# Performance work log

Measured on AMD Instinct MI355X. Metric: run time of the kernel, lower is better.

Reference implementation:

```python
import jax, jax.numpy as jnp
import numpy as np

N = 200000
B = 2
GX, GY, GZ = 480, 360, 32          # full-res voxel grid for input_coords
GX2, GY2, GZ2 = 240, 180, 16       # output_scale grid for bxyz_indx
CIN, CR, COUT = 64, 64, 64
CR2 = CR // 2
P_SCALE = (2, 4, 6, 8)


def setup_inputs() -> dict:
    key = jax.random.key(0)
    ks = jax.random.split(key, 24)
    s = 0.05
    input_data = jax.random.normal(ks[0], (N, CIN), dtype=jnp.float32)
    bcol = jax.random.randint(ks[1], (N, 1), 0, B, dtype=jnp.int32)
    xc = jax.random.randint(ks[2], (N, 1), 0, GX, dtype=jnp.int32)
    yc = jax.random.randint(ks[3], (N, 1), 0, GY, dtype=jnp.int32)
    zc = jax.random.randint(ks[4], (N, 1), 0, GZ, dtype=jnp.int32)
    input_coords = jnp.concatenate([bcol, xc, yc, zc], axis=1)
    input_coords_inv = jax.random.randint(ks[5], (N,), 0, N, dtype=jnp.int32)
    b2 = jax.random.randint(ks[6], (N, 1), 0, B, dtype=jnp.int32)
    x2 = jax.random.randint(ks[7], (N, 1), 0, GX2, dtype=jnp.int32)
    y2 = jax.random.randint(ks[8], (N, 1), 0, GY2, dtype=jnp.int32)
    z2 = jax.random.randint(ks[9], (N, 1), 0, GZ2, dtype=jnp.int32)
    bxyz_indx = jnp.concatenate([b2, x2, y2, z2], axis=1)
    # parameters (torch Linear stored here as [in, out])
    W_red = jax.random.normal(ks[10], (CIN, CR)) * s
    b_red = jnp.zeros((CR,), jnp.float32)
    fc_list_W = jax.random.normal(ks[11], (4, CR, CR2)) * s
    fc_list_b = jnp.zeros((4, CR2), jnp.float32)
    fcs_W = jax.random.normal(ks[12], (4, CR2, CR2)) * s
    fcs_b = jnp.zeros((4, CR2), jnp.float32)
    fc_W = jax.random.normal(ks[13], (CR2, CR2)) * s
    out_fc_W = jax.random.normal(ks[14], (CR2, CR)) * s
    lo_W1 = jax.random.normal(ks[15], (2 * CR, CR)) * s
    lo_W2 = jax.random.normal(ks[16], (CR, COUT)) * s
    lo_b2 = jnp.zeros((COUT,), jnp.float32)
    return dict(input_data=input_data, input_coords=input_coords,
                input_coords_inv=input_coords_inv, bxyz_indx=bxyz_indx,
                W_red=W_red, b_red=b_red, fc_list_W=fc_list_W, fc_list_b=fc_list_b,
                fcs_W=fcs_W, fcs_b=fcs_b, fc_W=fc_W, out_fc_W=out_fc_W,
                lo_W1=lo_W1, lo_W2=lo_W2, lo_b2=lo_b2)


def _segment_mean(x, seg, num_segments):
    sums = jax.ops.segment_sum(x, seg, num_segments=num_segments)
    cnt = jax.ops.segment_sum(jnp.ones((x.shape[0], 1), x.dtype), seg,
                              num_segments=num_segments)
    return sums / jnp.maximum(cnt, 1.0)


def reference(input_data, input_coords, input_coords_inv, bxyz_indx,
              W_red, b_red, fc_list_W, fc_list_b, fcs_W, fcs_b,
              fc_W, out_fc_W, lo_W1, lo_W2, lo_b2):
    reduced = jax.nn.relu(input_data @ W_red + b_red)          # [N, CR]
    bcol = input_coords[:, 0]
    xyz = input_coords[:, 1:]
    outs = []
    for j, ps in enumerate(P_SCALE):
        dx = (GX - 1) // ps + 1
        dy = (GY - 1) // ps + 1
        dz = (GZ - 1) // ps + 1
        q = xyz // ps                                          # [N, 3]
        # dense linearized voxel id replaces torch.unique(return_inverse)
        lin = ((bcol * dx + q[:, 0]) * dy + q[:, 1]) * dz + q[:, 2]
        nseg = B * dx * dy * dz
        fkm = _segment_mean(reduced, lin, nseg)                # [nseg, CR]
        att = jax.nn.relu(fkm @ fc_list_W[j] + fc_list_b[j])   # [nseg, CR2]
        outs.append(att[lin])                                  # gather back [N, CR2]
    scale_features = jnp.stack(outs, axis=1)                   # [N, 4, CR2]
    feat_S = scale_features.sum(axis=1)                        # [N, CR2]
    feat_Z = jax.nn.relu(feat_S @ fc_W)                        # [N, CR2]
    att_v = jax.nn.sigmoid(jnp.einsum('nc,kcd->nkd', feat_Z, fcs_W) + fcs_b)
    fused = (scale_features * att_v).sum(axis=1) @ out_fc_W    # [N, CR]
    output_f = jnp.concatenate([reduced, fused], axis=1)       # [N, 2*CR]
    proj = jax.nn.relu(output_f @ lo_W1) @ lo_W2 + lo_b2       # [N, COUT]
    proj = proj[input_coords_inv]
    # with_fm branch: index = (b, z, y, x) of bxyz_indx (b,x,y,z)
    lin2 = ((bxyz_indx[:, 0] * GZ2 + bxyz_indx[:, 3]) * GY2
            + bxyz_indx[:, 2]) * GX2 + bxyz_indx[:, 1]
    tv_fmap = jax.ops.segment_max(proj, lin2, num_segments=B * GZ2 * GY2 * GX2)
    tv_fmap = jnp.where(jnp.isneginf(tv_fmap), 0.0, tv_fmap)   # empty voxels -> 0
    return proj, tv_fmap, lin2
```

## Files before the change

### kernel.cpp

```cpp
#include <hip/hip_runtime.h>
#include <math.h>

#define NPTS   200000
#define CR     64
#define CR2    32

#define NSEG0      1382400
#define SUM123_ROW2 172800
#define SUM123_ROW3 230400
#define SUM123_ROWS 252000

#define TVSEG  1382400
#define GX2    240
#define GY2    180
#define GZ2    16

#define NBATCH 21600

__device__ __forceinline__ float bcastf(float v, int l) {
    return __int_as_float(__builtin_amdgcn_readlane(__float_as_int(v), l));
}

__device__ __forceinline__ int lin_scale(int b, int x, int y, int z,
                                         int ps, int dx, int dy, int dz) {
    int qx = x / ps, qy = y / ps, qz = z / ps;
    return ((b * dx + qx) * dy + qy) * dz + qz;
}

__device__ __forceinline__ void seg_decode(int seg, int& l1, int& l2, int& l3) {
    int qz = seg & 15; int rest = seg >> 4;
    int qy = rest % 180; int rest2 = rest / 180;
    int qx = rest2 % 240; int bb = rest2 / 240;
    l1 = ((bb * 120 + (qx >> 1)) * 90 + (qy >> 1)) * 8 + (qz >> 1);
    l2 = ((bb *  80 + (qx / 3)) * 60 + (qy / 3)) * 6 + (qz / 3);
    l3 = ((bb *  60 + (qx >> 2)) * 45 + (qy >> 2)) * 4 + (qz >> 2);
}

__device__ __forceinline__ int gatt_child(int s, int lane) {
    if (s < SUM123_ROW2) {
        int qz = s & 7, t = s >> 3;
        int qy = t % 90, t2 = t / 90;
        int qx = t2 % 120, b = t2 / 120;
        if (lane >= 8) return -1;
        int i = (lane >> 2) & 1, j = (lane >> 1) & 1, k = lane & 1;
        return ((b * 240 + 2 * qx + i) * 180 + 2 * qy + j) * 16 + 2 * qz + k;
    } else if (s < SUM123_ROW3) {
        int s2 = s - SUM123_ROW2;
        int qz = s2 % 6, t = s2 / 6;
        int qy = t % 60, t2 = t / 60;
        int qx = t2 % 80, b = t2 / 80;
        if (lane >= 27) return -1;
        int i = lane / 9, j = (lane / 3) % 3, k = lane % 3;
        int cz = 3 * qz + k;
        if (cz >= 16) return -1;
        return ((b * 240 + 3 * qx + i) * 180 + 3 * qy + j) * 16 + cz;
    } else {
        int s3 = s - SUM123_ROW3;
        int qz = s3 & 3, t = s3 >> 2;
        int qy = t % 45, t2 = t / 45;
        int qx = t2 % 60, b = t2 / 60;
        int i = lane >> 4, j = (lane >> 2) & 3, k = lane & 3;
        return ((b * 240 + 4 * qx + i) * 180 + 4 * qy + j) * 16 + 4 * qz + k;
    }
}

__global__ __launch_bounds__(256) void k_redscat(
        const float* __restrict__ in, const int* __restrict__ coords,
        const float* __restrict__ Wred, const float* __restrict__ bred,
        float* __restrict__ red, float* __restrict__ sum0,
        float* __restrict__ cnt) {
    __shared__ float Wl[CR * CR];
    for (int i = threadIdx.x; i < CR * CR; i += blockDim.x) Wl[i] = Wred[i];
    __syncthreads();
    int lane = threadIdx.x & 63;
    float bl = bred[lane];
    int wid  = blockIdx.x * 4 + (threadIdx.x >> 6);
    int nw   = gridDim.x * 4;
    for (int p = wid; p < NPTS / 2; p += nw) {
        int r0 = 2 * p, r1 = r0 + 1;
        float x0 = in[(size_t)r0 * CR + lane];
        float x1 = in[(size_t)r1 * CR + lane];
        float acc0 = bl, acc1 = bl;
#pragma unroll
        for (int k = 0; k < CR; ++k) {
            float w = Wl[k * CR + lane];
            acc0 += bcastf(x0, k) * w;
            acc1 += bcastf(x1, k) * w;
        }
        acc0 = fmaxf(acc0, 0.f); acc1 = fmaxf(acc1, 0.f);
        red[(size_t)r0 * CR + lane] = acc0;
        red[(size_t)r1 * CR + lane] = acc1;
        int4 c0 = ((const int4*)coords)[r0];
        int4 c1 = ((const int4*)coords)[r1];
        int l0a = lin_scale(c0.x, c0.y, c0.z, c0.w, 2, 240, 180, 16);
        int l0b = lin_scale(c1.x, c1.y, c1.z, c1.w, 2, 240, 180, 16);
        atomicAdd(&sum0[(size_t)l0a * CR + lane], acc0);
        atomicAdd(&sum0[(size_t)l0b * CR + lane], acc1);
        if (lane == 0) {
            atomicAdd(&cnt[l0a], 1.0f);
            atomicAdd(&cnt[l0b], 1.0f);
        }
    }
}

__global__ __launch_bounds__(256) void k_gatt(
        const float* __restrict__ sum0, float* __restrict__ attbuf,
        const float* __restrict__ cnt,
        const float* __restrict__ fcW, const float* __restrict__ fcB,
        int* __restrict__ list0, int* __restrict__ listCount,
        int* __restrict__ rankArr,
        const float* __restrict__ outW, const float* __restrict__ loW1,
        float* __restrict__ M) {
    __shared__ float sw[3 * CR * CR2];
    __shared__ int s_wavecnt[4];
    __shared__ int s_base;

    if (blockIdx.x < 8) {
        int e = blockIdx.x * 256 + threadIdx.x;
        if (e < 2048) {
            int r = e >> 6, c = e & 63;
            float acc = 0.f;
#pragma unroll
            for (int k = 0; k < 64; ++k)
                acc += outW[r * 64 + k] * loW1[(64 + k) * 64 + c];
            M[e] = acc;
        }
        return;
    }
    if (blockIdx.x < 1088) {
        int lane = threadIdx.x & 63;
        int w = threadIdx.x >> 6;
        int batch0 = (blockIdx.x - 8) * 20 + w * 5;
        int mycount = 0;
        for (int b = 0; b < 5; ++b) {
            float c = cnt[(batch0 + b) * 64 + lane];
            unsigned long long mask = __ballot(c > 0.f);
            mycount += __popcll(mask);
        }
        if (lane == 0) s_wavecnt[w] = mycount;
        __syncthreads();
        if (threadIdx.x == 0) {
            int tot = s_wavecnt[0] + s_wavecnt[1] + s_wavecnt[2] + s_wavecnt[3];
            s_base = atomicAdd(listCount, tot);
        }
        __syncthreads();
        int offset = s_base;
        for (int ww = 0; ww < w; ++ww) offset += s_wavecnt[ww];
        for (int b = 0; b < 5; ++b) {
            int cell = (batch0 + b) * 64 + lane;
            float c = cnt[cell];
            unsigned long long mask = __ballot(c > 0.f);
            if (c > 0.f) {
                int my = offset + __popcll(mask & ((1ull << lane) - 1ull));
                list0[my] = cell;
                rankArr[cell] = my;
            }
            offset += __popcll(mask);
        }
        return;
    }

    for (int i = threadIdx.x; i < 3 * CR * CR2; i += blockDim.x)
        sw[i] = fcW[CR * CR2 + i];
    __syncthreads();
    int lane = threadIdx.x & 63;
    int d = lane & 31;
    int wid = (blockIdx.x - 1088) * 4 + (threadIdx.x >> 6);
    int nw  = 2048 * 4;
    for (int p = wid; p < SUM123_ROWS / 2; p += nw) {
        int s0 = 2 * p, s1 = s0 + 1;
        const float* w; float bj;
        if (s0 < SUM123_ROW2)      { w = sw;        bj = fcB[1 * CR2 + d]; }
        else if (s0 < SUM123_ROW3) { w = sw + 2048; bj = fcB[2 * CR2 + d]; }
        else                       { w = sw + 4096; bj = fcB[3 * CR2 + d]; }

        int cl0 = gatt_child(s0, lane);
        int cl1 = gatt_child(s1, lane);
        float c0 = (cl0 >= 0) ? cnt[cl0] : 0.f;
        float c1 = (cl1 >= 0) ? cnt[cl1] : 0.f;
        unsigned long long mask0 = __ballot(c0 > 0.f);
        unsigned long long mask1 = __ballot(c1 > 0.f);
        if (!(mask0 | mask1)) continue;
        float t0 = c0, t1 = c1;
#pragma unroll
        for (int sh = 1; sh <= 32; sh <<= 1) {
            t0 += __shfl_xor(t0, sh, 64);
            t1 += __shfl_xor(t1, sh, 64);
        }

        float acc0 = 0.f, acc1 = 0.f;
        if (s0 < SUM123_ROW2) {
            int qz = s0 & 7, t = s0 >> 3;
            int qy = t % 90, t2 = t / 90;
            int qx = t2 % 120, b = t2 / 120;
            int base0 = ((b * 240 + 2 * qx) * 180 + 2 * qy) * 16 + 2 * qz;
            int base1 = base0 + 2;
#pragma unroll
            for (int c = 0; c < 8; ++c) {
                int off = (c >> 2) * 2880 + ((c >> 1) & 1) * 16 + (c & 1);
                if (mask0 & (1ull << c)) acc0 += sum0[(size_t)(base0 + off) * CR + lane];
                if (mask1 & (1ull << c)) acc1 += sum0[(size_t)(base1 + off) * CR + lane];
            }
        } else if (s0 < SUM123_ROW3) {
            int s2 = s0 - SUM123_ROW2;
            int qz = s2 % 6, t = s2 / 6;
            int qy = t % 60, t2 = t / 60;
            int qx = t2 % 80, b = t2 / 80;
            int base0 = ((b * 240 + 3 * qx) * 180 + 3 * qy) * 16 + 3 * qz;
            int base1 = base0 + 3;
#pragma unroll
            for (int c = 0; c < 27; ++c) {
                int off = (c / 9) * 2880 + ((c / 3) % 3) * 16 + (c % 3);
                if (mask0 & (1ull << c)) acc0 += sum0[(size_t)(base0 + off) * CR + lane];
                if (mask1 & (1ull << c)) acc1 += sum0[(size_t)(base1 + off) * CR + lane];
            }
        } else {
            int s3 = s0 - SUM123_ROW3;
            int qz = s3 & 3, t = s3 >> 2;
            int qy = t % 45, t2 = t / 45;
            int qx = t2 % 60, b = t2 / 60;
            int base0 = ((b * 240 + 4 * qx) * 180 + 4 * qy) * 16 + 4 * qz;
            int base1 = base0 + 4;
#pragma unroll
            for (int c = 0; c < 64; ++c) {
                int off = (c >> 4) * 2880 + ((c >> 2) & 3) * 16 + (c & 3);
                if (mask0 & (1ull << c)) acc0 += sum0[(size_t)(base0 + off) * CR + lane];
                if (mask1 & (1ull << c)) acc1 += sum0[(size_t)(base1 + off) * CR + lane];
            }
        }

        float m0 = acc0 * (1.f / fmaxf(t0, 1.f));
        float m1 = acc1 * (1.f / fmaxf(t1, 1.f));
        float p0 = bj, p1 = bj;
#pragma unroll
        for (int k = 0; k < CR; ++k) {
            float wk = w[k * CR2 + d];
            p0 += bcastf(m0, k) * wk;
            p1 += bcastf(m1, k) * wk;
        }
        float a0 = fmaxf(p0, 0.f), a1 = fmaxf(p1, 0.f);
        if (lane < 32) attbuf[(size_t)s0 * CR2 + lane] = a0;
        else           attbuf[(size_t)s1 * CR2 + d]    = a1;
    }
}

__global__ __launch_bounds__(256) void k_segf(
        float* __restrict__ tv, const float* __restrict__ cnt,
        const int* __restrict__ list0, const int* __restrict__ listCount,
        const float* __restrict__ fcW, const float* __restrict__ fcB,
        const float* __restrict__ fc_W, const float* __restrict__ fcsW,
        const float* __restrict__ fcsB, const float* __restrict__ M,
        const float* __restrict__ attbuf, float* __restrict__ gc) {
    __shared__ float s_w0[2048];
    __shared__ float s_fcZ[1024];
    __shared__ float s_fcs[4096];
    __shared__ float s_M[2048];
    for (int i = threadIdx.x; i < 2048; i += 256) s_w0[i]  = fcW[i];
    for (int i = threadIdx.x; i < 1024; i += 256) s_fcZ[i] = fc_W[i];
    for (int i = threadIdx.x; i < 4096; i += 256) s_fcs[i] = fcsW[i];
    for (int i = threadIdx.x; i < 2048; i += 256) s_M[i]   = M[i];
    __syncthreads();

    int lane = threadIdx.x & 63;
    int d = lane & 31;
    int h = lane >> 5;
    float b0  = fcB[d];
    float vbA = fcsB[(h ? 1 : 0) * CR2 + d];
    float vbB = fcsB[(h ? 3 : 2) * CR2 + d];
    const float* VA = s_fcs + (h ? 1 : 0) * 1024;
    const float* VB = s_fcs + (h ? 3 : 2) * 1024;

    int total = listCount[0];
    int ngroups = (total + 3) >> 2;
    int wid = blockIdx.x * 4 + (threadIdx.x >> 6);
    int nw  = gridDim.x * 4;
    for (int g = wid; g < ngroups; g += nw) {
        int r0 = 4 * g;
        int r1 = min(r0 + 1, total - 1);
        int r2 = min(r0 + 2, total - 1);
        int r3 = min(r0 + 3, total - 1);
        int seg0 = list0[r0], seg1 = list0[r1], seg2 = list0[r2], seg3 = list0[r3];
        float* row0 = tv + (size_t)seg0 * CR;
        float* row1 = tv + (size_t)seg1 * CR;
        float* row2 = tv + (size_t)seg2 * CR;
        float* row3 = tv + (size_t)seg3 * CR;
        float m0 = row0[lane] * (1.f / cnt[seg0]);
        float m1 = row1[lane] * (1.f / cnt[seg1]);
        float m2 = row2[lane] * (1.f / cnt[seg2]);
        float m3 = row3[lane] * (1.f / cnt[seg3]);
        row0[lane] = 0.f; row1[lane] = 0.f; row2[lane] = 0.f; row3[lane] = 0.f;

        float p0 = b0, p1 = b0, p2 = b0, p3 = b0;
#pragma unroll
        for (int k = 0; k < CR; ++k) {
            float wk = s_w0[k * CR2 + d];
            p0 += bcastf(m0, k) * wk;
            p1 += bcastf(m1, k) * wk;
            p2 += bcastf(m2, k) * wk;
            p3 += bcastf(m3, k) * wk;
        }
        float a0_0 = fmaxf(p0, 0.f), a0_1 = fmaxf(p1, 0.f);
        float a0_2 = fmaxf(p2, 0.f), a0_3 = fmaxf(p3, 0.f);

        int l1_0, l2_0, l3_0, l1_1, l2_1, l3_1;
        int l1_2, l2_2, l3_2, l1_3, l2_3, l3_3;
        seg_decode(seg0, l1_0, l2_0, l3_0);
        seg_decode(seg1, l1_1, l2_1, l3_1);
        seg_decode(seg2, l1_2, l2_2, l3_2);
        seg_decode(seg3, l1_3, l2_3, l3_3);

        float a1_0 = attbuf[(size_t)l1_0 * CR2 + d];
        float a2_0 = attbuf[(size_t)(SUM123_ROW2 + l2_0) * CR2 + d];
        float a3_0 = attbuf[(size_t)(SUM123_ROW3 + l3_0) * CR2 + d];
        float a1_1 = attbuf[(size_t)l1_1 * CR2 + d];
        float a2_1 = attbuf[(size_t)(SUM123_ROW2 + l2_1) * CR2 + d];
        float a3_1 = attbuf[(size_t)(SUM123_ROW3 + l3_1) * CR2 + d];
        float a1_2 = attbuf[(size_t)l1_2 * CR2 + d];
        float a2_2 = attbuf[(size_t)(SUM123_ROW2 + l2_2) * CR2 + d];
        float a3_2 = attbuf[(size_t)(SUM123_ROW3 + l3_2) * CR2 + d];
        float a1_3 = attbuf[(size_t)l1_3 * CR2 + d];
        float a2_3 = attbuf[(size_t)(SUM123_ROW2 + l2_3) * CR2 + d];
        float a3_3 = attbuf[(size_t)(SUM123_ROW3 + l3_3) * CR2 + d];

        float fS0 = a0_0 + a1_0 + a2_0 + a3_0;
        float fS1 = a0_1 + a1_1 + a2_1 + a3_1;
        float fS2 = a0_2 + a1_2 + a2_2 + a3_2;
        float fS3 = a0_3 + a1_3 + a2_3 + a3_3;

        float z0 = 0.f, z1 = 0.f, z2 = 0.f, z3 = 0.f;
#pragma unroll
        for (int cc = 0; cc < CR2; ++cc) {
            float wz = s_fcZ[cc * CR2 + d];
            z0 += bcastf(fS0, cc) * wz;
            z1 += bcastf(fS1, cc) * wz;
            z2 += bcastf(fS2, cc) * wz;
            z3 += bcastf(fS3, cc) * wz;
        }
        float fZ0 = fmaxf(z0, 0.f), fZ1 = fmaxf(z1, 0.f);
        float fZ2 = fmaxf(z2, 0.f), fZ3 = fmaxf(z3, 0.f);

        float avA0 = vbA, avA1 = vbA, avA2 = vbA, avA3 = vbA;
        float avB0 = vbB, avB1 = vbB, avB2 = vbB, avB3 = vbB;
#pragma unroll
        for (int cc = 0; cc < CR2; ++cc) {
            float wa = VA[cc * CR2 + d];
            float wb = VB[cc * CR2 + d];
            float f0 = bcastf(fZ0, cc), f1 = bcastf(fZ1, cc);
            float f2 = bcastf(fZ2, cc), f3 = bcastf(fZ3, cc);
            avA0 += f0 * wa; avB0 += f0 * wb;
            avA1 += f1 * wa; avB1 += f1 * wb;
            avA2 += f2 * wa; avB2 += f2 * wb;
            avA3 += f3 * wa; avB3 += f3 * wb;
        }
        avA0 = 1.f / (1.f + __expf(-avA0)); avB0 = 1.f / (1.f + __expf(-avB0));
        avA1 = 1.f / (1.f + __expf(-avA1)); avB1 = 1.f / (1.f + __expf(-avB1));
        avA2 = 1.f / (1.f + __expf(-avA2)); avB2 = 1.f / (1.f + __expf(-avB2));
        avA3 = 1.f / (1.f + __expf(-avA3)); avB3 = 1.f / (1.f + __expf(-avB3));

        float u0 = (h ? a1_0 : a0_0) * avA0 + (h ? a3_0 : a2_0) * avB0;
        float u1 = (h ? a1_1 : a0_1) * avA1 + (h ? a3_1 : a2_1) * avB1;
        float u2 = (h ? a1_2 : a0_2) * avA2 + (h ? a3_2 : a2_2) * avB2;
        float u3 = (h ? a1_3 : a0_3) * avA3 + (h ? a3_3 : a2_3) * avB3;
        float fI0 = u0 + __shfl_xor(u0, 32, 64);
        float fI1 = u1 + __shfl_xor(u1, 32, 64);
        float fI2 = u2 + __shfl_xor(u2, 32, 64);
        float fI3 = u3 + __shfl_xor(u3, 32, 64);

        float g0 = 0.f, g1 = 0.f, g2 = 0.f, g3 = 0.f;
#pragma unroll
        for (int dd = 0; dd < CR2; ++dd) {
            float wm = s_M[dd * CR + lane];
            g0 += bcastf(fI0, dd) * wm;
            g1 += bcastf(fI1, dd) * wm;
            g2 += bcastf(fI2, dd) * wm;
            g3 += bcastf(fI3, dd) * wm;
        }
        gc[(size_t)r0 * CR + lane] = g0;
        gc[(size_t)r1 * CR + lane] = g1;
        gc[(size_t)r2 * CR + lane] = g2;
        gc[(size_t)r3 * CR + lane] = g3;
    }
}

__device__ __forceinline__ unsigned int fkey(float f) {
    unsigned int b = __float_as_uint(f);
    return (b & 0x80000000u) ? ~b : (b | 0x80000000u);
}

__global__ __launch_bounds__(256) void k_pgmax(
        const float* __restrict__ red, const float* __restrict__ gc,
        const int* __restrict__ rankArr,
        const int* __restrict__ coords, const int* __restrict__ inv,
        const int* __restrict__ bxyz,
        const float* __restrict__ loW1, const float* __restrict__ loW2,
        const float* __restrict__ lob2, float* __restrict__ outProj,
        float* __restrict__ outLin, unsigned int* __restrict__ tvKey,
        unsigned char* __restrict__ flags) {
    __shared__ float s_W1[4096];
    __shared__ float s_W2[4096];
    for (int i = threadIdx.x; i < 4096; i += 256) s_W1[i] = loW1[i];
    for (int i = threadIdx.x; i < 4096; i += 256) s_W2[i] = loW2[i];
    __syncthreads();

    int lane = threadIdx.x & 63;
    float lob = lob2[lane];
    int wid = blockIdx.x * 4 + (threadIdx.x >> 6);
    int nw  = gridDim.x * 4;
    for (int q = wid; q < NPTS / 4; q += nw) {
        int i0 = 4 * q, i1 = i0 + 1, i2 = i0 + 2, i3 = i0 + 3;
        int s0 = inv[i0], s1 = inv[i1], s2 = inv[i2], s3 = inv[i3];
        int4 c0 = ((const int4*)coords)[s0];
        int4 c1 = ((const int4*)coords)[s1];
        int4 c2 = ((const int4*)coords)[s2];
        int4 c3 = ((const int4*)coords)[s3];
        int l0 = lin_scale(c0.x, c0.y, c0.z, c0.w, 2, 240, 180, 16);
        int l1 = lin_scale(c1.x, c1.y, c1.z, c1.w, 2, 240, 180, 16);
        int l2 = lin_scale(c2.x, c2.y, c2.z, c2.w, 2, 240, 180, 16);
        int l3 = lin_scale(c3.x, c3.y, c3.z, c3.w, 2, 240, 180, 16);
        int rk0 = rankArr[l0], rk1 = rankArr[l1];
        int rk2 = rankArr[l2], rk3 = rankArr[l3];

        int4 b0 = ((const int4*)bxyz)[i0];
        int4 b1 = ((const int4*)bxyz)[i1];
        int4 b2 = ((const int4*)bxyz)[i2];
        int4 b3 = ((const int4*)bxyz)[i3];
        int n0 = ((b0.x * GZ2 + b0.w) * GY2 + b0.z) * GX2 + b0.y;
        int n1 = ((b1.x * GZ2 + b1.w) * GY2 + b1.z) * GX2 + b1.y;
        int n2 = ((b2.x * GZ2 + b2.w) * GY2 + b2.z) * GX2 + b2.y;
        int n3 = ((b3.x * GZ2 + b3.w) * GY2 + b3.z) * GX2 + b3.y;
        if (lane == 0) {
            outLin[i0] = (float)n0; flags[n0] = 1;
            outLin[i1] = (float)n1; flags[n1] = 1;
            outLin[i2] = (float)n2; flags[n2] = 1;
            outLin[i3] = (float)n3; flags[n3] = 1;
        }

        float x0 = red[(size_t)s0 * CR + lane];
        float x1 = red[(size_t)s1 * CR + lane];
        float x2 = red[(size_t)s2 * CR + lane];
        float x3 = red[(size_t)s3 * CR + lane];
        float h0 = gc[(size_t)rk0 * CR + lane];
        float h1 = gc[(size_t)rk1 * CR + lane];
        float h2 = gc[(size_t)rk2 * CR + lane];
        float h3 = gc[(size_t)rk3 * CR + lane];
#pragma unroll
        for (int k = 0; k < CR; ++k) {
            float w = s_W1[k * CR + lane];
            h0 += bcastf(x0, k) * w;
            h1 += bcastf(x1, k) * w;
            h2 += bcastf(x2, k) * w;
            h3 += bcastf(x3, k) * w;
        }
        h0 = fmaxf(h0, 0.f); h1 = fmaxf(h1, 0.f);
        h2 = fmaxf(h2, 0.f); h3 = fmaxf(h3, 0.f);

        float q0 = lob, q1 = lob, q2 = lob, q3 = lob;
#pragma unroll
        for (int k = 0; k < CR; ++k) {
            float w = s_W2[k * CR + lane];
            q0 += bcastf(h0, k) * w;
            q1 += bcastf(h1, k) * w;
            q2 += bcastf(h2, k) * w;
            q3 += bcastf(h3, k) * w;
        }
        outProj[(size_t)i0 * CR + lane] = q0;
        outProj[(size_t)i1 * CR + lane] = q1;
        outProj[(size_t)i2 * CR + lane] = q2;
        outProj[(size_t)i3 * CR + lane] = q3;

        atomicMax(&tvKey[(size_t)n0 * CR + lane], fkey(q0));
        atomicMax(&tvKey[(size_t)n1 * CR + lane], fkey(q1));
        atomicMax(&tvKey[(size_t)n2 * CR + lane], fkey(q2));
        atomicMax(&tvKey[(size_t)n3 * CR + lane], fkey(q3));
    }
}

__global__ __launch_bounds__(256) void k_fix(
        unsigned int* __restrict__ tv, const unsigned char* __restrict__ flags) {
    int lane = threadIdx.x & 63;
    int wid = blockIdx.x * 4 + (threadIdx.x >> 6);
    int nw  = gridDim.x * 4;
    for (int batch = wid; batch < NBATCH; batch += nw) {
        int base = batch * 64;
        unsigned char f = flags[base + lane];
        unsigned long long mask = __ballot(f != 0);
        while (mask) {
            int j = __ffsll((long long)mask) - 1; mask &= mask - 1;
            size_t idx = (size_t)(base + j) * CR + lane;
            unsigned int k = tv[idx];
            float v = (k == 0u) ? 0.f
                    : __uint_as_float((k & 0x80000000u) ? (k & 0x7FFFFFFFu) : ~k);
            ((float*)tv)[idx] = v;
        }
    }
}

extern "C" void kernel_launch(void* const* d_in, const int* in_sizes, int n_in,
                              void* d_out, int out_size, void* d_ws, size_t ws_size,
                              hipStream_t stream) {
    (void)in_sizes; (void)n_in; (void)out_size; (void)ws_size;
    const float* in_data = (const float*)d_in[0];
    const int*   coords  = (const int*)d_in[1];
    const int*   inv     = (const int*)d_in[2];
    const int*   bxyz    = (const int*)d_in[3];
    const float* W_red   = (const float*)d_in[4];
    const float* b_red   = (const float*)d_in[5];
    const float* fcW     = (const float*)d_in[6];
    const float* fcB     = (const float*)d_in[7];
    const float* fcsW    = (const float*)d_in[8];
    const float* fcsB    = (const float*)d_in[9];
    const float* fc_W    = (const float*)d_in[10];
    const float* outW    = (const float*)d_in[11];
    const float* loW1    = (const float*)d_in[12];
    const float* loW2    = (const float*)d_in[13];
    const float* lob2    = (const float*)d_in[14];

    float* outProj = (float*)d_out;
    float* tv      = outProj + (size_t)NPTS * CR;
    float* outLin  = tv + (size_t)TVSEG * CR;

    float* ws_f   = (float*)d_ws;
    float* red    = ws_f;
    float* attbuf = red + (size_t)NPTS * CR;
    float* cnt    = attbuf + (size_t)SUM123_ROWS * CR2;
    int*   listCount = (int*)(cnt + (size_t)NSEG0);
    unsigned char* flags = (unsigned char*)(listCount + 4);
    int*   rankArr   = (int*)(flags + (size_t)TVSEG);
    int*   list0     = rankArr + (size_t)NSEG0;
    float* gc     = (float*)(list0 + (size_t)NPTS);
    float* Mmat   = gc + (size_t)NPTS * CR;

    hipMemsetAsync(tv, 0, (size_t)TVSEG * CR * sizeof(float), stream);
    hipMemsetAsync(cnt, 0, (size_t)NSEG0 * 4 + 16 + (size_t)TVSEG, stream);

    k_redscat<<<2048, 256, 0, stream>>>(in_data, coords, W_red, b_red,
                                        red, tv, cnt);
    k_gatt<<<3136, 256, 0, stream>>>(tv, attbuf, cnt, fcW, fcB,
                                     list0, listCount, rankArr,
                                     outW, loW1, Mmat);
    k_segf<<<2048, 256, 0, stream>>>(tv, cnt, list0, (const int*)listCount,
                                     fcW, fcB, fc_W, fcsW, fcsB, Mmat,
                                     attbuf, gc);
    k_pgmax<<<2048, 256, 0, stream>>>(red, gc, rankArr, coords, inv, bxyz,
                                      loW1, loW2, lob2, outProj,
                                      outLin, (unsigned int*)tv, flags);
    k_fix<<<2048, 256, 0, stream>>>((unsigned int*)tv, flags);
}
```

Before: 1.037 ms.

## Precompute per-point rank in segf side blocks and prefetch inv in pgmax

Adds extra blocks to k_segf that compute each point's scale-2 segment rank (coords to lin to rankArr) into a ptRank array. k_pgmax then does one indirect load per point instead of a coords gather plus a rankArr gather. It also software-prefetches the next int4 of inv and moves the red and ptRank loads earlier, deferring the gc add until after the first matvec. This shortens the dependent-load chain in pgmax at the cost of extra blocks and a small extra workspace array.

```diff
diff --git a/kernel.cpp b/kernel.cpp
--- a/kernel.cpp
+++ b/kernel.cpp
@@ -16,6 +16,7 @@
 #define GZ2    16
 
 #define NBATCH 21600
+#define SEGF_MAIN 2048
 
 __device__ __forceinline__ float bcastf(float v, int l) {
     return __int_as_float(__builtin_amdgcn_readlane(__float_as_int(v), l));
@@ -250,7 +251,18 @@
         const float* __restrict__ fcW, const float* __restrict__ fcB,
         const float* __restrict__ fc_W, const float* __restrict__ fcsW,
         const float* __restrict__ fcsB, const float* __restrict__ M,
-        const float* __restrict__ attbuf, float* __restrict__ gc) {
+        const float* __restrict__ attbuf, float* __restrict__ gc,
+        const int* __restrict__ coords, const int* __restrict__ rankArr,
+        int* __restrict__ ptRank) {
+    if (blockIdx.x >= SEGF_MAIN) {
+        int idx = (blockIdx.x - SEGF_MAIN) * 256 + threadIdx.x;
+        if (idx < NPTS) {
+            int4 c = ((const int4*)coords)[idx];
+            int l = lin_scale(c.x, c.y, c.z, c.w, 2, 240, 180, 16);
+            ptRank[idx] = rankArr[l];
+        }
+        return;
+    }
     __shared__ float s_w0[2048];
     __shared__ float s_fcZ[1024];
     __shared__ float s_fcs[4096];
@@ -273,7 +285,7 @@
     int total = listCount[0];
     int ngroups = (total + 3) >> 2;
     int wid = blockIdx.x * 4 + (threadIdx.x >> 6);
-    int nw  = gridDim.x * 4;
+    int nw  = SEGF_MAIN * 4;
     for (int g = wid; g < ngroups; g += nw) {
         int r0 = 4 * g;
         int r1 = min(r0 + 1, total - 1);
@@ -389,9 +401,8 @@
 
 __global__ __launch_bounds__(256) void k_pgmax(
         const float* __restrict__ red, const float* __restrict__ gc,
-        const int* __restrict__ rankArr,
-        const int* __restrict__ coords, const int* __restrict__ inv,
-        const int* __restrict__ bxyz,
+        const int* __restrict__ ptRank,
+        const int* __restrict__ inv, const int* __restrict__ bxyz,
         const float* __restrict__ loW1, const float* __restrict__ loW2,
         const float* __restrict__ lob2, float* __restrict__ outProj,
         float* __restrict__ outLin, unsigned int* __restrict__ tvKey,
@@ -406,19 +417,25 @@
     float lob = lob2[lane];
     int wid = blockIdx.x * 4 + (threadIdx.x >> 6);
     int nw  = gridDim.x * 4;
-    for (int q = wid; q < NPTS / 4; q += nw) {
+    const int NQ = NPTS / 4;
+
+    int q = wid;
+    int4 sv = make_int4(0, 0, 0, 0);
+    if (q < NQ) sv = ((const int4*)inv)[q];
+    for (; q < NQ; q += nw) {
+        int qn = q + nw;
+        int4 svn = sv;
+        if (qn < NQ) svn = ((const int4*)inv)[qn];
+
         int i0 = 4 * q, i1 = i0 + 1, i2 = i0 + 2, i3 = i0 + 3;
-        int s0 = inv[i0], s1 = inv[i1], s2 = inv[i2], s3 = inv[i3];
-        int4 c0 = ((const int4*)coords)[s0];
-        int4 c1 = ((const int4*)coords)[s1];
-        int4 c2 = ((const int4*)coords)[s2];
-        int4 c3 = ((const int4*)coords)[s3];
-        int l0 = lin_scale(c0.x, c0.y, c0.z, c0.w, 2, 240, 180, 16);
-        int l1 = lin_scale(c1.x, c1.y, c1.z, c1.w, 2, 240, 180, 16);
-        int l2 = lin_scale(c2.x, c2.y, c2.z, c2.w, 2, 240, 180, 16);
-        int l3 = lin_scale(c3.x, c3.y, c3.z, c3.w, 2, 240, 180, 16);
-        int rk0 = rankArr[l0], rk1 = rankArr[l1];
-        int rk2 = rankArr[l2], rk3 = rankArr[l3];
+        int s0 = sv.x, s1 = sv.y, s2 = sv.z, s3 = sv.w;
+
+        int rk0 = ptRank[s0], rk1 = ptRank[s1];
+        int rk2 = ptRank[s2], rk3 = ptRank[s3];
+        float x0 = red[(size_t)s0 * CR + lane];
+        float x1 = red[(size_t)s1 * CR + lane];
+        float x2 = red[(size_t)s2 * CR + lane];
+        float x3 = red[(size_t)s3 * CR + lane];
 
         int4 b0 = ((const int4*)bxyz)[i0];
         int4 b1 = ((const int4*)bxyz)[i1];
@@ -435,14 +452,12 @@
             outLin[i3] = (float)n3; flags[n3] = 1;
         }
 
-        float x0 = red[(size_t)s0 * CR + lane];
-        float x1 = red[(size_t)s1 * CR + lane];
-        float x2 = red[(size_t)s2 * CR + lane];
-        float x3 = red[(size_t)s3 * CR + lane];
-        float h0 = gc[(size_t)rk0 * CR + lane];
-        float h1 = gc[(size_t)rk1 * CR + lane];
-        float h2 = gc[(size_t)rk2 * CR + lane];
-        float h3 = gc[(size_t)rk3 * CR + lane];
+        float g0r = gc[(size_t)rk0 * CR + lane];
+        float g1r = gc[(size_t)rk1 * CR + lane];
+        float g2r = gc[(size_t)rk2 * CR + lane];
+        float g3r = gc[(size_t)rk3 * CR + lane];
+
+        float h0 = 0.f, h1 = 0.f, h2 = 0.f, h3 = 0.f;
 #pragma unroll
         for (int k = 0; k < CR; ++k) {
             float w = s_W1[k * CR + lane];
@@ -451,8 +466,8 @@
             h2 += bcastf(x2, k) * w;
             h3 += bcastf(x3, k) * w;
         }
-        h0 = fmaxf(h0, 0.f); h1 = fmaxf(h1, 0.f);
-        h2 = fmaxf(h2, 0.f); h3 = fmaxf(h3, 0.f);
+        h0 = fmaxf(h0 + g0r, 0.f); h1 = fmaxf(h1 + g1r, 0.f);
+        h2 = fmaxf(h2 + g2r, 0.f); h3 = fmaxf(h3 + g3r, 0.f);
 
         float q0 = lob, q1 = lob, q2 = lob, q3 = lob;
 #pragma unroll
@@ -472,6 +487,8 @@
         atomicMax(&tvKey[(size_t)n1 * CR + lane], fkey(q1));
         atomicMax(&tvKey[(size_t)n2 * CR + lane], fkey(q2));
         atomicMax(&tvKey[(size_t)n3 * CR + lane], fkey(q3));
+
+        sv = svn;
     }
 }
 
@@ -529,6 +546,7 @@
     int*   list0     = rankArr + (size_t)NSEG0;
     float* gc     = (float*)(list0 + (size_t)NPTS);
     float* Mmat   = gc + (size_t)NPTS * CR;
+    int*   ptRank = (int*)(Mmat + 2048);
 
     hipMemsetAsync(tv, 0, (size_t)TVSEG * CR * sizeof(float), stream);
     hipMemsetAsync(cnt, 0, (size_t)NSEG0 * 4 + 16 + (size_t)TVSEG, stream);
@@ -538,10 +556,10 @@
     k_gatt<<<3136, 256, 0, stream>>>(tv, attbuf, cnt, fcW, fcB,
                                      list0, listCount, rankArr,
                                      outW, loW1, Mmat);
-    k_segf<<<2048, 256, 0, stream>>>(tv, cnt, list0, (const int*)listCount,
+    k_segf<<<SEGF_MAIN + 784, 256, 0, stream>>>(tv, cnt, list0, (const int*)listCount,
                                      fcW, fcB, fc_W, fcsW, fcsB, Mmat,
-                                     attbuf, gc);
-    k_pgmax<<<2048, 256, 0, stream>>>(red, gc, rankArr, coords, inv, bxyz,
+                                     attbuf, gc, coords, rankArr, ptRank);
+    k_pgmax<<<2048, 256, 0, stream>>>(red, gc, ptRank, inv, bxyz,
                                       loW1, loW2, lob2, outProj,
                                       outLin, (unsigned int*)tv, flags);
     k_fix<<<2048, 256, 0, stream>>>((unsigned int*)tv, flags);
```

Result: slower. 1.062 ms (+2.4%).
